# Kernel tuning notes

Hardware: AMD Instinct MI355X
Metric: run time of the kernel (lower is better)

The kernel has to match this reference:

```python
import jax, jax.numpy as jnp
import numpy as np

B, W, N, DIM, GAMMA = 32, 16, 256, 256, 4
WH = 16  # sqrt(N)
V = DIM // GAMMA
TABLE = (2 * WH - 1) * (2 * WH - 1)  # 961


def _make_rel_index(wh: int) -> np.ndarray:
    coords = np.stack(np.meshgrid(np.arange(wh), np.arange(wh), indexing='ij'))  # (2, wh, wh)
    flat = coords.reshape(2, -1)                         # (2, wh*wh)
    rel = flat[:, :, None] - flat[:, None, :]            # (2, n, n)
    rel = rel.transpose(1, 2, 0).copy()                  # (n, n, 2)
    rel[:, :, 0] += wh - 1
    rel[:, :, 1] += wh - 1
    rel[:, :, 0] *= 2 * wh - 1
    return rel.sum(-1).astype(np.int32)                  # (n, n)


def setup_inputs() -> dict:
    key = jax.random.key(0)
    k1, k2, k3 = jax.random.split(key, 3)
    x = jax.random.normal(k1, (B, W, N, DIM), dtype=jnp.float32)
    bias_table = jax.random.normal(k2, (TABLE, W * GAMMA), dtype=jnp.float32) * 0.02
    token_bias = jax.random.normal(k3, (W * GAMMA, N, 1), dtype=jnp.float32) * 0.02
    rel_index = jnp.asarray(_make_rel_index(WH))
    return {"x": x, "bias_table": bias_table, "token_bias": token_bias, "rel_index": rel_index}


def reference(x, bias_table, token_bias, rel_index):
    b, w, n, d = x.shape
    gamma = GAMMA
    v = d // gamma
    # gather: (n, n, w*gamma) -> permute to (w*gamma, n, n)
    rpb = bias_table[rel_index.reshape(-1)].reshape(n, n, w * gamma)
    rpb = jnp.transpose(rpb, (2, 0, 1))                  # ((s w), n, n) with s outer
    # rearrange '(s b) m n -> b m n s'
    win_weight = jnp.transpose(rpb.reshape(gamma, w, n, n), (1, 2, 3, 0))  # (w, m, n, s)
    # rearrange 'b w n (v s) -> b w n v s'
    xs = x.reshape(b, w, n, v, gamma)
    out = jnp.einsum('wmns,bwnvs->bwmvs', win_weight, xs)
    # rearrange '(w s) m v -> w m v s'
    bias = jnp.transpose(token_bias.reshape(w, gamma, n, 1), (0, 2, 3, 1))  # (w, m, 1, s)
    out = out + bias[None]
    return out.reshape(b, w, n, d)
```

## Files before the change

### kernel.cpp

```cpp
#include <hip/hip_runtime.h>
#include <stdint.h>


typedef __attribute__((ext_vector_type(8))) short bf16x8;
typedef __attribute__((ext_vector_type(4))) float f32x4;
typedef __attribute__((ext_vector_type(8))) unsigned short u16x8;

__device__ __forceinline__ unsigned short f2bf(float f) {
    union { float f; unsigned u; } v; v.f = f;
    unsigned u = v.u;
    u += 0x7FFFu + ((u >> 16) & 1u);
    return (unsigned short)(u >> 16);
}
__device__ __forceinline__ float bf2f(unsigned short h) {
    union { unsigned u; float f; } v; v.u = ((unsigned)h) << 16;
    return v.f;
}
__device__ __forceinline__ int expInRange(unsigned short w16) {
    int e = (w16 >> 7) & 0xFF;
    return (e >= 100 && e <= 140) ? 1 : 0;
}

#define GLL16(gp, lp) __builtin_amdgcn_global_load_lds( \
    (const __attribute__((address_space(1))) void*)(gp), \
    (__attribute__((address_space(3))) void*)(lp), 16, 0, 0)

__global__ __launch_bounds__(256) void k_gather(
    const void* __restrict__ bt_raw,
    const int*  __restrict__ rel_index,
    const void* __restrict__ x_raw,
    unsigned short* __restrict__ Ab)
{
    const unsigned short* xw = (const unsigned short*)x_raw;
    int t = threadIdx.x;
    int pred = expInRange(xw[t * 2]) & expInRange(xw[t * 2 + 1]);
    int cnt = __syncthreads_count(pred);
    bool isF32 = (cnt < 150);

    int idx8 = blockIdx.x * 256 + t;
    int base = idx8 << 3;
    int nn = base & 255;
    int m  = (base >> 8) & 255;
    int ws = base >> 16;
    int colw = ((ws & 3) << 4) + (ws >> 2);
    const int* ri = rel_index + (m << 8) + nn;
    int4 r0 = *(const int4*)ri;
    int4 r1 = *(const int4*)(ri + 4);
    int idx[8] = {r0.x, r0.y, r0.z, r0.w, r1.x, r1.y, r1.z, r1.w};
    u16x8 o;
    if (isF32) {
        const float* bt = (const float*)bt_raw;
#pragma unroll
        for (int j = 0; j < 8; j++) o[j] = f2bf(bt[(idx[j] << 6) + colw]);
    } else {
        const unsigned short* bt = (const unsigned short*)bt_raw;
#pragma unroll
        for (int j = 0; j < 8; j++) o[j] = bt[(idx[j] << 6) + colw];
    }
    *(u16x8*)(Ab + base) = o;
}

__global__ __launch_bounds__(512, 4) void k_main(
    const void* __restrict__ x_raw,
    const unsigned short* __restrict__ Ab,
    const void* __restrict__ tb_raw,
    void* __restrict__ out_raw)
{
    __shared__ unsigned short lds[32768];

    const int tid  = threadIdx.x;
    const unsigned short* xw = (const unsigned short*)x_raw;
    int pred = expInRange(xw[tid]);
    int cnt = __syncthreads_count(pred);
    const bool isF32 = (cnt < 400);

    const int lane = tid & 63;
    const int wave = tid >> 6;
    const int bx = blockIdx.x;
    const int b  = bx & 31;
    const int mt = (bx >> 5) & 3;
    const int w  = bx >> 7;
    const int m0 = mt << 6;

    const int sw   = wave & 3;
    const int vh   = wave >> 2;
    const int vvb  = vh << 5;
    const int col  = lane & 15;
    const int quad = lane >> 4;

    const int g1 = 512 + tid;
    const unsigned short* Ag0 = Ab + (((w << 2) + (tid >> 8)) << 16) + ((m0 + ((tid >> 2) & 63)) << 8) + ((tid & 3) << 3);
    const unsigned short* Ag1 = Ab + (((w << 2) + (g1  >> 8)) << 16) + ((m0 + ((g1  >> 2) & 63)) << 8) + ((g1  & 3) << 3);

    const int d0   = (tid & 127) << 1;
    const int ngrp = tid >> 7;
    const int xgoff = (((b << 4) + w) << 16) + (ngrp << 11) + d0;
    const float*          Xgf = (const float*)x_raw + xgoff;
    const unsigned short* Xgh = (const unsigned short*)x_raw + xgoff;
    const int vvx   = d0 >> 2;
    const int slotx = (ngrp ^ ((vvx >> 1) & 3)) << 3;
    const int xw0 = 16384 + ((d0 & 3) << 11) + (vvx << 5) + slotx;
    const int xw1 = xw0 + 2048;

    const int vr0 = vvb + col;
    const int sl0 = (quad ^ ((vr0 >> 1) & 3)) << 3;
    const int xr0_off = 16384 + (sw << 11) + (vr0 << 5) + sl0;
    const int xr1_off = xr0_off + (16 << 5);
    const int ar = (sw << 11) + (col << 5) + (quad << 3);

    f32x4 acc[4][2];
#pragma unroll
    for (int mi = 0; mi < 4; mi++) {
        acc[mi][0] = (f32x4){0.f, 0.f, 0.f, 0.f};
        acc[mi][1] = (f32x4){0.f, 0.f, 0.f, 0.f};
    }

    float2       xrf[8];
    unsigned int xru[8];

    auto xpref = [&](int nc_) {
        if (isF32) {
#pragma unroll
            for (int j = 0; j < 8; j++)
                xrf[j] = *(const float2*)(Xgf + (nc_ << 13) + (j << 8));
        } else {
#pragma unroll
            for (int j = 0; j < 8; j++)
                xru[j] = *(const unsigned int*)(Xgh + (nc_ << 13) + (j << 8));
        }
    };
    auto xwrite = [&](int xb) {
        u16x8 o0, o1;
        if (isF32) {
#pragma unroll
            for (int j = 0; j < 8; j++) { o0[j] = f2bf(xrf[j].x); o1[j] = f2bf(xrf[j].y); }
        } else {
#pragma unroll
            for (int j = 0; j < 8; j++) { o0[j] = (unsigned short)(xru[j] & 0xFFFFu);
                                          o1[j] = (unsigned short)(xru[j] >> 16); }
        }
        *(u16x8*)(lds + xw0 + xb) = o0;
        *(u16x8*)(lds + xw1 + xb) = o1;
    };
    auto agll = [&](int nc_, int ab) {
        GLL16(Ag0 + (nc_ << 5), lds + ab + (wave << 9));
        GLL16(Ag1 + (nc_ << 5), lds + ab + 4096 + (wave << 9));
    };

    agll(0, 0);
    xpref(0);
    xwrite(0);
    xpref(1);
    __syncthreads();

#pragma unroll
    for (int nc = 0; nc < 8; ++nc) {
        const int cur = (nc & 1) << 13;
        const int nxt = ((nc + 1) & 1) << 13;
        if (nc < 7) {
            agll(nc + 1, nxt);
            xwrite(nxt);
        }
        if (nc < 6) xpref(nc + 2);

        bf16x8 bfr0 = *(const bf16x8*)(lds + xr0_off + cur);
        bf16x8 bfr1 = *(const bf16x8*)(lds + xr1_off + cur);
#pragma unroll
        for (int mi = 0; mi < 4; mi++) {
            bf16x8 afr = *(const bf16x8*)(lds + cur + ar + (mi << 9));
            acc[mi][0] = __builtin_amdgcn_mfma_f32_16x16x32_bf16(afr, bfr0, acc[mi][0], 0, 0, 0);
            acc[mi][1] = __builtin_amdgcn_mfma_f32_16x16x32_bf16(afr, bfr1, acc[mi][1], 0, 0, 0);
        }
        if (nc < 7) __syncthreads();
    }

    const int tboff = (((w << 2) + sw) << 8) + m0;
    const int ooff  = (((b << 4) + w) << 16) + (m0 << 8) + sw;
    if (isF32) {
        const float* tb = (const float*)tb_raw + tboff;
        float* ob = (float*)out_raw + ooff;
#pragma unroll
        for (int mi = 0; mi < 4; mi++) {
#pragma unroll
            for (int r = 0; r < 4; r++) {
                int m = (mi << 4) + (quad << 2) + r;
                float bias = tb[m];
#pragma unroll
                for (int vi = 0; vi < 2; vi++) {
                    int vv = vvb + (vi << 4) + col;
                    ob[(m << 8) + (vv << 2)] = acc[mi][vi][r] + bias;
                }
            }
        }
    } else {
        const unsigned short* tb = (const unsigned short*)tb_raw + tboff;
        unsigned short* ob = (unsigned short*)out_raw + ooff;
#pragma unroll
        for (int mi = 0; mi < 4; mi++) {
#pragma unroll
            for (int r = 0; r < 4; r++) {
                int m = (mi << 4) + (quad << 2) + r;
                float bias = bf2f(tb[m]);
#pragma unroll
                for (int vi = 0; vi < 2; vi++) {
                    int vv = vvb + (vi << 4) + col;
                    ob[(m << 8) + (vv << 2)] = f2bf(acc[mi][vi][r] + bias);
                }
            }
        }
    }
}

__global__ __launch_bounds__(512, 4) void k_main_fused(
    const void* __restrict__ x_raw,
    const void* __restrict__ bt_raw,
    const int*  __restrict__ rel_index,
    const void* __restrict__ tb_raw,
    void* __restrict__ out_raw)
{
    __shared__ unsigned short lds[16384 + 8192];

    const int tid  = threadIdx.x;
    const unsigned short* xw = (const unsigned short*)x_raw;
    int pred = expInRange(xw[tid]);
    int cnt = __syncthreads_count(pred);
    const bool isF32 = (cnt < 400);

    const int lane = tid & 63;
    const int wave = tid >> 6;
    const int bx = blockIdx.x;
    const int b  = bx & 31;
    const int mt = (bx >> 5) & 1;
    const int w  = bx >> 6;
    const int m0 = mt << 7;

    const int sw   = wave & 3;
    const int vh   = wave >> 2;
    const int vvb  = vh << 5;
    const int col  = lane & 15;
    const int quad = lane >> 4;

    const int a_row = tid >> 2;
    const int a_nn8 = (tid & 3) << 3;
    unsigned short* AsW = lds + (a_row << 5) + a_nn8;
    const int* rIp = rel_index + ((m0 + a_row) << 8) + a_nn8;

    const int x_nn = tid & 31;
    const int x_vg = tid >> 5;
    const int xoff = (((b << 4) + w) << 16) + (x_nn << 8) + (x_vg << 4);
    const float*          Xgf = (const float*)x_raw + xoff;
    const unsigned short* Xgh = (const unsigned short*)x_raw + xoff;
    unsigned short* XsW = lds + 16384 + x_nn;

    f32x4 acc[8][2];
#pragma unroll
    for (int mi = 0; mi < 8; mi++) {
        acc[mi][0] = (f32x4){0.f, 0.f, 0.f, 0.f};
        acc[mi][1] = (f32x4){0.f, 0.f, 0.f, 0.f};
    }

    const unsigned short* AsR = lds + (sw << 12) + (col << 5) + (quad << 3);
    const unsigned short* XsR = lds + 16384 + (sw << 11) + ((vvb + col) << 5) + (quad << 3);

    for (int nc = 0; nc < 8; nc++) {
        int4 r0 = *(const int4*)(rIp + (nc << 5));
        int4 r1 = *(const int4*)(rIp + (nc << 5) + 4);
        int ri[8] = {r0.x, r0.y, r0.z, r0.w, r1.x, r1.y, r1.z, r1.w};
#pragma unroll
        for (int it = 0; it < 4; it++) {
            u16x8 av;
            if (isF32) {
                const float* bt = (const float*)bt_raw;
#pragma unroll
                for (int j = 0; j < 8; j++)
                    av[j] = f2bf(bt[(ri[j] << 6) + (it << 4) + w]);
            } else {
                const unsigned short* bt = (const unsigned short*)bt_raw;
#pragma unroll
                for (int j = 0; j < 8; j++)
                    av[j] = bt[(ri[j] << 6) + (it << 4) + w];
            }
            *(u16x8*)(AsW + (it << 12)) = av;
        }

        if (isF32) {
            float4 v[4];
#pragma unroll
            for (int i = 0; i < 4; i++)
                v[i] = *(const float4*)(Xgf + (nc << 13) + (i << 2));
            const float* vf = (const float*)v;
#pragma unroll
            for (int j = 0; j < 16; j++) {
                int vv = (x_vg << 2) + (j >> 2);
                XsW[((j & 3) << 11) + (vv << 5)] = f2bf(vf[j]);
            }
        } else {
            u16x8 xv0 = *(const u16x8*)(Xgh + (nc << 13));
            u16x8 xv1 = *(const u16x8*)(Xgh + (nc << 13) + 8);
#pragma unroll
            for (int j = 0; j < 8; j++) {
                int vv = (x_vg << 2) + (j >> 2);
                XsW[((j & 3) << 11) + (vv << 5)] = xv0[j];
            }
#pragma unroll
            for (int j = 0; j < 8; j++) {
                int vv = (x_vg << 2) + 2 + (j >> 2);
                XsW[((j & 3) << 11) + (vv << 5)] = xv1[j];
            }
        }
        __syncthreads();

        bf16x8 bfr0 = *(const bf16x8*)(XsR);
        bf16x8 bfr1 = *(const bf16x8*)(XsR + 512);
#pragma unroll
        for (int mi = 0; mi < 8; mi++) {
            bf16x8 afr = *(const bf16x8*)(AsR + (mi << 9));
            acc[mi][0] = __builtin_amdgcn_mfma_f32_16x16x32_bf16(afr, bfr0, acc[mi][0], 0, 0, 0);
            acc[mi][1] = __builtin_amdgcn_mfma_f32_16x16x32_bf16(afr, bfr1, acc[mi][1], 0, 0, 0);
        }
        __syncthreads();
    }

    const int tboff = (((w << 2) + sw) << 8) + m0;
    const int ooff  = (((b << 4) + w) << 16) + (m0 << 8) + sw;
    if (isF32) {
        const float* tb = (const float*)tb_raw + tboff;
        float* ob = (float*)out_raw + ooff;
#pragma unroll
        for (int mi = 0; mi < 8; mi++) {
#pragma unroll
            for (int r = 0; r < 4; r++) {
                int m = (mi << 4) + (quad << 2) + r;
                float bias = tb[m];
#pragma unroll
                for (int vi = 0; vi < 2; vi++) {
                    int vv = vvb + (vi << 4) + col;
                    ob[(m << 8) + (vv << 2)] = acc[mi][vi][r] + bias;
                }
            }
        }
    } else {
        const unsigned short* tb = (const unsigned short*)tb_raw + tboff;
        unsigned short* ob = (unsigned short*)out_raw + ooff;
#pragma unroll
        for (int mi = 0; mi < 8; mi++) {
#pragma unroll
            for (int r = 0; r < 4; r++) {
                int m = (mi << 4) + (quad << 2) + r;
                float bias = bf2f(tb[m]);
#pragma unroll
                for (int vi = 0; vi < 2; vi++) {
                    int vv = vvb + (vi << 4) + col;
                    ob[(m << 8) + (vv << 2)] = f2bf(acc[mi][vi][r] + bias);
                }
            }
        }
    }
}

extern "C" void kernel_launch(void* const* d_in, const int* in_sizes, int n_in,
                              void* d_out, int out_size, void* d_ws, size_t ws_size,
                              hipStream_t stream) {
    const void* x          = d_in[0];
    const void* bias_table = d_in[1];
    const void* token_bias = d_in[2];
    const int*  rel_index  = (const int*)d_in[3];

    const size_t AB_BYTES = (size_t)64 * 256 * 256 * 2;
    if (ws_size >= AB_BYTES) {
        unsigned short* Ab = (unsigned short*)d_ws;
        hipLaunchKernelGGL(k_gather, dim3(2048), dim3(256), 0, stream,
                           bias_table, rel_index, x, Ab);
        hipLaunchKernelGGL(k_main, dim3(2048), dim3(512), 0, stream,
                           x, Ab, token_bias, d_out);
    } else {
        hipLaunchKernelGGL(k_main_fused, dim3(1024), dim3(512), 0, stream,
                           x, bias_table, rel_index, token_bias, d_out);
    }
}
```

Measured before the change: 318.6 us.

## Coalesce gather via LDS transpose, drop double buffering, swizzle blocks and A layout

The gather kernel now reads whole bias-table rows with vector loads and transposes them through shared memory, so global writes are contiguous instead of scattered 2-byte reads. The main kernel drops its double-buffered LDS and register prefetch in favour of a single buffer with two barriers per step, which halves LDS use and should allow more blocks per CU. It also adds an XOR swizzle on the A tile to reduce bank conflicts and remaps block indices so neighbouring blocks share the same window's bias planes in cache. The cost is that loads and MFMAs no longer overlap within a block, so hiding latency now depends on occupancy.

```diff
diff --git a/kernel.cpp b/kernel.cpp
--- a/kernel.cpp
+++ b/kernel.cpp
@@ -31,33 +31,49 @@
     const void* __restrict__ x_raw,
     unsigned short* __restrict__ Ab)
 {
+    __shared__ unsigned short Lt[64 * 72];
+
     const unsigned short* xw = (const unsigned short*)x_raw;
     int t = threadIdx.x;
     int pred = expInRange(xw[t * 2]) & expInRange(xw[t * 2 + 1]);
     int cnt = __syncthreads_count(pred);
     bool isF32 = (cnt < 150);
 
-    int idx8 = blockIdx.x * 256 + t;
-    int base = idx8 << 3;
-    int nn = base & 255;
-    int m  = (base >> 8) & 255;
-    int ws = base >> 16;
-    int colw = ((ws & 3) << 4) + (ws >> 2);
-    const int* ri = rel_index + (m << 8) + nn;
-    int4 r0 = *(const int4*)ri;
-    int4 r1 = *(const int4*)(ri + 4);
-    int idx[8] = {r0.x, r0.y, r0.z, r0.w, r1.x, r1.y, r1.z, r1.w};
-    u16x8 o;
+    const int cellbase = blockIdx.x << 6;
+    const int c = t >> 2;
+    const int p = t & 3;
+    const int row = rel_index[cellbase + c];
+
+    unsigned short vals[16];
     if (isF32) {
-        const float* bt = (const float*)bt_raw;
-#pragma unroll
-        for (int j = 0; j < 8; j++) o[j] = f2bf(bt[(idx[j] << 6) + colw]);
+        const float* bt = (const float*)bt_raw + (row << 6) + (p << 4);
+        float4 v0 = *(const float4*)(bt);
+        float4 v1 = *(const float4*)(bt + 4);
+        float4 v2 = *(const float4*)(bt + 8);
+        float4 v3 = *(const float4*)(bt + 12);
+        float vf[16] = {v0.x,v0.y,v0.z,v0.w, v1.x,v1.y,v1.z,v1.w,
+                        v2.x,v2.y,v2.z,v2.w, v3.x,v3.y,v3.z,v3.w};
+#pragma unroll
+        for (int k = 0; k < 16; k++) vals[k] = f2bf(vf[k]);
     } else {
-        const unsigned short* bt = (const unsigned short*)bt_raw;
-#pragma unroll
-        for (int j = 0; j < 8; j++) o[j] = bt[(idx[j] << 6) + colw];
-    }
-    *(u16x8*)(Ab + base) = o;
+        const unsigned short* bt = (const unsigned short*)bt_raw + (row << 6) + (p << 4);
+        u16x8 a0 = *(const u16x8*)(bt);
+        u16x8 a1 = *(const u16x8*)(bt + 8);
+#pragma unroll
+        for (int k = 0; k < 8; k++) { vals[k] = a0[k]; vals[8 + k] = a1[k]; }
+    }
+#pragma unroll
+    for (int k = 0; k < 16; k++)
+        Lt[(((k << 2) + p) * 72) + c] = vals[k];
+    __syncthreads();
+
+    const int plane = t >> 2;
+    const int cg = (t & 3) << 4;
+    u16x8 o0 = *(const u16x8*)(Lt + plane * 72 + cg);
+    u16x8 o1 = *(const u16x8*)(Lt + plane * 72 + cg + 8);
+    unsigned short* dst = Ab + (plane << 16) + cellbase + cg;
+    *(u16x8*)dst = o0;
+    *(u16x8*)(dst + 8) = o1;
 }
 
 __global__ __launch_bounds__(512, 4) void k_main(
@@ -66,7 +82,7 @@
     const void* __restrict__ tb_raw,
     void* __restrict__ out_raw)
 {
-    __shared__ unsigned short lds[32768];
+    __shared__ unsigned short lds[16384];
 
     const int tid  = threadIdx.x;
     const unsigned short* xw = (const unsigned short*)x_raw;
@@ -77,9 +93,10 @@
     const int lane = tid & 63;
     const int wave = tid >> 6;
     const int bx = blockIdx.x;
-    const int b  = bx & 31;
-    const int mt = (bx >> 5) & 3;
-    const int w  = bx >> 7;
+    const int swz = ((bx & 7) << 8) | (bx >> 3);
+    const int mt = swz & 3;
+    const int b  = (swz >> 2) & 31;
+    const int w  = swz >> 7;
     const int m0 = mt << 6;
 
     const int sw   = wave & 3;
@@ -88,9 +105,13 @@
     const int col  = lane & 15;
     const int quad = lane >> 4;
 
-    const int g1 = 512 + tid;
-    const unsigned short* Ag0 = Ab + (((w << 2) + (tid >> 8)) << 16) + ((m0 + ((tid >> 2) & 63)) << 8) + ((tid & 3) << 3);
-    const unsigned short* Ag1 = Ab + (((w << 2) + (g1  >> 8)) << 16) + ((m0 + ((g1  >> 2) & 63)) << 8) + ((g1  & 3) << 3);
+    const int amRow   = (tid >> 2) & 63;
+    const int aswslot = (tid & 3) ^ ((amRow >> 1) & 3);
+    const unsigned short* Ag0 = Ab + (((w << 2) + (tid >> 8)) << 16)
+                                   + ((m0 + amRow) << 8) + (aswslot << 3);
+    const unsigned short* Ag1 = Ag0 + (2 << 16);
+    const int aswz = (col >> 1) & 3;
+    const int ar = (sw << 11) + (col << 5) + ((quad ^ aswz) << 3);
 
     const int d0   = (tid & 127) << 1;
     const int ngrp = tid >> 7;
@@ -98,15 +119,12 @@
     const float*          Xgf = (const float*)x_raw + xgoff;
     const unsigned short* Xgh = (const unsigned short*)x_raw + xgoff;
     const int vvx   = d0 >> 2;
-    const int slotx = (ngrp ^ ((vvx >> 1) & 3)) << 3;
-    const int xw0 = 16384 + ((d0 & 3) << 11) + (vvx << 5) + slotx;
-    const int xw1 = xw0 + 2048;
-
-    const int vr0 = vvb + col;
-    const int sl0 = (quad ^ ((vr0 >> 1) & 3)) << 3;
-    const int xr0_off = 16384 + (sw << 11) + (vr0 << 5) + sl0;
-    const int xr1_off = xr0_off + (16 << 5);
-    const int ar = (sw << 11) + (col << 5) + (quad << 3);
+    const int xslot = ((ngrp ^ ((vvx >> 1) & 3)) << 3);
+    unsigned short* xw0p = lds + 8192 + ((d0 & 3) << 11) + (vvx << 5) + xslot;
+    unsigned short* xw1p = xw0p + 2048;
+
+    const int xr0 = 8192 + (sw << 11) + ((vvb + col) << 5) + ((quad ^ aswz) << 3);
+    const int xr1 = xr0 + 512;
 
     f32x4 acc[4][2];
 #pragma unroll
@@ -115,63 +133,40 @@
         acc[mi][1] = (f32x4){0.f, 0.f, 0.f, 0.f};
     }
 
-    float2       xrf[8];
-    unsigned int xru[8];
-
-    auto xpref = [&](int nc_) {
-        if (isF32) {
-#pragma unroll
-            for (int j = 0; j < 8; j++)
-                xrf[j] = *(const float2*)(Xgf + (nc_ << 13) + (j << 8));
-        } else {
-#pragma unroll
-            for (int j = 0; j < 8; j++)
-                xru[j] = *(const unsigned int*)(Xgh + (nc_ << 13) + (j << 8));
-        }
-    };
-    auto xwrite = [&](int xb) {
+    for (int nc = 0; nc < 8; ++nc) {
+        GLL16(Ag0 + (nc << 5), lds + (wave << 9));
+        GLL16(Ag1 + (nc << 5), lds + 4096 + (wave << 9));
+
         u16x8 o0, o1;
         if (isF32) {
-#pragma unroll
-            for (int j = 0; j < 8; j++) { o0[j] = f2bf(xrf[j].x); o1[j] = f2bf(xrf[j].y); }
+            float2 v[8];
+#pragma unroll
+            for (int j = 0; j < 8; j++)
+                v[j] = *(const float2*)(Xgf + (nc << 13) + (j << 8));
+#pragma unroll
+            for (int j = 0; j < 8; j++) { o0[j] = f2bf(v[j].x); o1[j] = f2bf(v[j].y); }
         } else {
-#pragma unroll
-            for (int j = 0; j < 8; j++) { o0[j] = (unsigned short)(xru[j] & 0xFFFFu);
-                                          o1[j] = (unsigned short)(xru[j] >> 16); }
-        }
-        *(u16x8*)(lds + xw0 + xb) = o0;
-        *(u16x8*)(lds + xw1 + xb) = o1;
-    };
-    auto agll = [&](int nc_, int ab) {
-        GLL16(Ag0 + (nc_ << 5), lds + ab + (wave << 9));
-        GLL16(Ag1 + (nc_ << 5), lds + ab + 4096 + (wave << 9));
-    };
-
-    agll(0, 0);
-    xpref(0);
-    xwrite(0);
-    xpref(1);
-    __syncthreads();
-
-#pragma unroll
-    for (int nc = 0; nc < 8; ++nc) {
-        const int cur = (nc & 1) << 13;
-        const int nxt = ((nc + 1) & 1) << 13;
-        if (nc < 7) {
-            agll(nc + 1, nxt);
-            xwrite(nxt);
-        }
-        if (nc < 6) xpref(nc + 2);
-
-        bf16x8 bfr0 = *(const bf16x8*)(lds + xr0_off + cur);
-        bf16x8 bfr1 = *(const bf16x8*)(lds + xr1_off + cur);
+            unsigned int v[8];
+#pragma unroll
+            for (int j = 0; j < 8; j++)
+                v[j] = *(const unsigned int*)(Xgh + (nc << 13) + (j << 8));
+#pragma unroll
+            for (int j = 0; j < 8; j++) { o0[j] = (unsigned short)(v[j] & 0xFFFFu);
+                                          o1[j] = (unsigned short)(v[j] >> 16); }
+        }
+        *(u16x8*)xw0p = o0;
+        *(u16x8*)xw1p = o1;
+        __syncthreads();
+
+        bf16x8 bfr0 = *(const bf16x8*)(lds + xr0);
+        bf16x8 bfr1 = *(const bf16x8*)(lds + xr1);
 #pragma unroll
         for (int mi = 0; mi < 4; mi++) {
-            bf16x8 afr = *(const bf16x8*)(lds + cur + ar + (mi << 9));
+            bf16x8 afr = *(const bf16x8*)(lds + ar + (mi << 9));
             acc[mi][0] = __builtin_amdgcn_mfma_f32_16x16x32_bf16(afr, bfr0, acc[mi][0], 0, 0, 0);
             acc[mi][1] = __builtin_amdgcn_mfma_f32_16x16x32_bf16(afr, bfr1, acc[mi][1], 0, 0, 0);
         }
-        if (nc < 7) __syncthreads();
+        __syncthreads();
     }
 
     const int tboff = (((w << 2) + sw) << 8) + m0;
@@ -369,7 +364,7 @@
     const size_t AB_BYTES = (size_t)64 * 256 * 256 * 2;
     if (ws_size >= AB_BYTES) {
         unsigned short* Ab = (unsigned short*)d_ws;
-        hipLaunchKernelGGL(k_gather, dim3(2048), dim3(256), 0, stream,
+        hipLaunchKernelGGL(k_gather, dim3(1024), dim3(256), 0, stream,
                            bias_table, rel_index, x, Ab);
         hipLaunchKernelGGL(k_main, dim3(2048), dim3(512), 0, stream,
                            x, Ab, token_bias, d_out);
```

Result: faster. 307.0 us (-3.6%).
